# Kernel optimization log

Measured on AMD Instinct MI355X. Metric: run time of the kernel, lower is better.

The kernel has to match this reference:

```python
import jax, jax.numpy as jnp
import numpy as np

N_NODES = 50000
N_EDGES = 400000
IN_DIM = 256
HIDDEN = 256
HEADS = 8
DPH = HIDDEN // HEADS  # 32, out_per_head
OUT_DIM = 128
SEG_EPS = 1e-12   # eps in _segment_softmax
BN_EPS = 1e-5     # torch BatchNorm1d default eps


def _xavier(key, shape):
    fan_in, fan_out = shape[0], shape[-1]
    lim = np.sqrt(6.0 / (fan_in + fan_out))
    return jax.random.uniform(key, shape, jnp.float32, -lim, lim)


def setup_inputs() -> dict:
    key = jax.random.key(0)
    ks = jax.random.split(key, 16)
    x = jax.random.normal(ks[0], (N_NODES, IN_DIM), jnp.float32)
    edge_index = jax.random.randint(ks[1], (2, N_EDGES), 0, N_NODES, jnp.int64)
    return {
        "x": x,
        "edge_index": edge_index,
        # layer 1
        "W1": _xavier(ks[2], (IN_DIM, HIDDEN)),
        "b1": jnp.zeros((HIDDEN,), jnp.float32),
        "a_l1": _xavier(ks[3], (HEADS, DPH)),
        "a_r1": _xavier(ks[4], (HEADS, DPH)),
        "g1": jnp.ones((HIDDEN,), jnp.float32),
        "be1": jnp.zeros((HIDDEN,), jnp.float32),
        # layer 2
        "W2": _xavier(ks[5], (HIDDEN, HIDDEN)),
        "b2": jnp.zeros((HIDDEN,), jnp.float32),
        "a_l2": _xavier(ks[6], (HEADS, DPH)),
        "a_r2": _xavier(ks[7], (HEADS, DPH)),
        "g2": jnp.ones((HIDDEN,), jnp.float32),
        "be2": jnp.zeros((HIDDEN,), jnp.float32),
        # classification head (mlp_hidden=0 -> single Linear)
        "Wh": _xavier(ks[8], (HIDDEN, OUT_DIM)),
        "bh": jnp.zeros((OUT_DIM,), jnp.float32),
    }


def _attn_aggregate(x_proj, src, dst, a_l, a_r):
    """Multi-head GAT aggregation, vectorized over heads.
    x_proj: [N, hidden]; src/dst: [E] int; a_l/a_r: [heads, dph]."""
    N = x_proj.shape[0]
    H = x_proj.reshape(N, HEADS, DPH)
    # per-node score halves (equivalent to (H[src]*a_l).sum + (H[dst]*a_r).sum)
    s_l = jnp.einsum('nhd,hd->nh', H, a_l)  # [N, heads]
    s_r = jnp.einsum('nhd,hd->nh', H, a_r)
    logits = s_l[src] + s_r[dst]            # [E, heads]
    # segment softmax exactly as the source: unstabilized exp + eps denom
    e = jnp.exp(logits)
    denom = jax.ops.segment_sum(e, dst, num_segments=N)       # [N, heads]
    alpha = e / (denom[dst] + SEG_EPS)                         # [E, heads]
    msg = H[src] * alpha[:, :, None]                           # [E, heads, dph]
    out = jax.ops.segment_sum(msg, dst, num_segments=N)        # [N, heads, dph]
    return out.reshape(N, HEADS * DPH)


def _batchnorm(h, gamma, beta):
    # training-mode BatchNorm1d: batch statistics, biased variance
    mean = h.mean(axis=0)
    var = h.var(axis=0)
    return (h - mean) * jax.lax.rsqrt(var + BN_EPS) * gamma + beta


def reference(x, edge_index, W1, b1, a_l1, a_r1, g1, be1,
              W2, b2, a_l2, a_r2, g2, be2, Wh, bh):
    N = x.shape[0]
    # symmetrize edges + add self loops
    ei = jnp.concatenate([edge_index, edge_index[::-1]], axis=1)
    loops = jnp.arange(N, dtype=ei.dtype)
    src = jnp.concatenate([ei[0], loops])
    dst = jnp.concatenate([ei[1], loops])

    x1 = x @ W1 + b1
    x1 = _attn_aggregate(x1, src, dst, a_l1, a_r1)
    x1 = jax.nn.relu(_batchnorm(x1, g1, be1))  # dropout = identity (eval)

    x2 = x1 @ W2 + b2
    x2 = _attn_aggregate(x2, src, dst, a_l2, a_r2)
    x2 = jax.nn.relu(_batchnorm(x2, g2, be2))

    logits = x2 @ Wh + bh  # [N, out_dim]
    return logits
```

## Files before the change

### kernel.cpp

```cpp
#include <hip/hip_runtime.h>
#include <hip/hip_bf16.h>
#include <math.h>

#define NN   50000
#define NE   400000
#define NE2  (2*NE + NN)
#define DIM  256
#define NH   8
#define NM   (NN*DIM)
#define NBLK 196
#define MPAD 50048

typedef __attribute__((ext_vector_type(8))) short bf16x8;
typedef __attribute__((ext_vector_type(4))) float f32x4;

#define GLOAD16(g, l) __builtin_amdgcn_global_load_lds( \
    (const __attribute__((address_space(1))) void*)(g), \
    (__attribute__((address_space(3))) void*)(l), 16, 0, 0)

__device__ __forceinline__ float b2f(unsigned short u) {
    unsigned int i = ((unsigned int)u) << 16;
    float f; __builtin_memcpy(&f, &i, 4); return f;
}
__device__ __forceinline__ unsigned short f2b(float f) {
    __hip_bfloat16 h = __float2bfloat16(f);
    unsigned short u; __builtin_memcpy(&u, &h, 2); return u;
}

__global__ __launch_bounds__(512) void gemm_bf16_wide(
    const unsigned short* __restrict__ A, const unsigned short* __restrict__ Bt,
    const float* __restrict__ bias, unsigned short* __restrict__ Cb)
{
    __shared__ short ldsA[4][128][8];
    __shared__ short ldsB[4][256][8];
    const int tid  = threadIdx.x;
    const int wave = tid >> 6, lane = tid & 63;
    const int wr = wave >> 2, wc = wave & 3;
    const int l15 = lane & 15, lk = lane >> 4;
    const int row0 = blockIdx.x * 128;

    f32x4 acc[4][4] = {};
    for (int k0 = 0; k0 < 256; k0 += 32) {
        GLOAD16(A + (size_t)(row0 + (tid & 127)) * 256 + k0 + (tid >> 7) * 8,
                &ldsA[tid >> 7][tid & 127][0]);
        #pragma unroll
        for (int c = 0; c < 2; ++c) {
            int idx = c * 512 + tid;
            int ch = idx >> 8, r = idx & 255;
            GLOAD16(Bt + (size_t)r * 256 + k0 + ch * 8, &ldsB[ch][r][0]);
        }
        __syncthreads();
        bf16x8 af[4], bf[4];
        #pragma unroll
        for (int m = 0; m < 4; ++m)
            af[m] = *reinterpret_cast<const bf16x8*>(&ldsA[lk][wr*64 + m*16 + l15][0]);
        #pragma unroll
        for (int n = 0; n < 4; ++n)
            bf[n] = *reinterpret_cast<const bf16x8*>(&ldsB[lk][wc*64 + n*16 + l15][0]);
        #pragma unroll
        for (int m = 0; m < 4; ++m)
            #pragma unroll
            for (int n = 0; n < 4; ++n)
                acc[m][n] = __builtin_amdgcn_mfma_f32_16x16x32_bf16(af[m], bf[n], acc[m][n], 0, 0, 0);
        __syncthreads();
    }
    #pragma unroll
    for (int m = 0; m < 4; ++m) {
        #pragma unroll
        for (int n = 0; n < 4; ++n) {
            int col = wc*64 + n*16 + l15;
            float bv = bias[col];
            #pragma unroll
            for (int r = 0; r < 4; ++r) {
                int row = row0 + wr*64 + m*16 + lk*4 + r;
                Cb[(size_t)row * 256 + col] = f2b(acc[m][n][r] + bv);
            }
        }
    }
}

__global__ __launch_bounds__(256) void gemm_bf16_head(
    const unsigned short* __restrict__ A, const unsigned short* __restrict__ Bt,
    const float* __restrict__ bias, float* __restrict__ C)
{
    __shared__ short ldsA[4][128][8];
    __shared__ short ldsB[4][128][8];
    const int tid  = threadIdx.x;
    const int wave = tid >> 6, lane = tid & 63;
    const int wr = wave >> 1, wc = wave & 1;
    const int l15 = lane & 15, lk = lane >> 4;
    const int row0 = blockIdx.x * 128;

    f32x4 acc[4][4] = {};
    for (int k0 = 0; k0 < 256; k0 += 32) {
        #pragma unroll
        for (int c = 0; c < 2; ++c) {
            int idx = c * 256 + tid;
            int ch = idx >> 7, r = idx & 127;
            GLOAD16(A  + (size_t)(row0 + r) * 256 + k0 + ch * 8, &ldsA[ch][r][0]);
            GLOAD16(Bt + (size_t)r * 256 + k0 + ch * 8, &ldsB[ch][r][0]);
        }
        __syncthreads();
        bf16x8 af[4], bf[4];
        #pragma unroll
        for (int m = 0; m < 4; ++m)
            af[m] = *reinterpret_cast<const bf16x8*>(&ldsA[lk][wr*64 + m*16 + l15][0]);
        #pragma unroll
        for (int n = 0; n < 4; ++n)
            bf[n] = *reinterpret_cast<const bf16x8*>(&ldsB[lk][wc*64 + n*16 + l15][0]);
        #pragma unroll
        for (int m = 0; m < 4; ++m)
            #pragma unroll
            for (int n = 0; n < 4; ++n)
                acc[m][n] = __builtin_amdgcn_mfma_f32_16x16x32_bf16(af[m], bf[n], acc[m][n], 0, 0, 0);
        __syncthreads();
    }
    #pragma unroll
    for (int m = 0; m < 4; ++m) {
        #pragma unroll
        for (int n = 0; n < 4; ++n) {
            int col = wc*64 + n*16 + l15;
            float bv = bias[col];
            #pragma unroll
            for (int r = 0; r < 4; ++r) {
                int row = row0 + wr*64 + m*16 + lk*4 + r;
                if (row < NN) C[(size_t)row * 128 + col] = acc[m][n][r] + bv;
            }
        }
    }
}

__global__ __launch_bounds__(256) void cast_x_bf16(
    const float* __restrict__ x, unsigned short* __restrict__ xb)
{
    int idx = blockIdx.x * 256 + threadIdx.x;
    if (idx >= NM / 4) return;
    float4 v = reinterpret_cast<const float4*>(x)[idx];
    ushort4 o = { f2b(v.x), f2b(v.y), f2b(v.z), f2b(v.w) };
    *reinterpret_cast<ushort4*>(&xb[(size_t)idx * 4]) = o;
}

__global__ __launch_bounds__(256) void cast_wt(
    const float* __restrict__ W, unsigned short* __restrict__ Wt, int K, int Nc)
{
    int i = blockIdx.x * 256 + threadIdx.x;
    if (i >= K * Nc) return;
    int k = i / Nc, n = i - k * Nc;
    Wt[n * K + k] = f2b(W[i]);
}

__global__ __launch_bounds__(256) void gat_scores_bf16(
    const unsigned short* __restrict__ Hb, const float* __restrict__ a_l,
    const float* __restrict__ a_r, float* __restrict__ el,
    float* __restrict__ er)
{
    const int wave = threadIdx.x >> 6;
    const int lane = threadIdx.x & 63;
    const int n = blockIdx.x * 4 + wave;
    if (n >= NN) return;
    const int c = lane * 4;
    const int h = lane >> 3;
    ushort4 hv = *reinterpret_cast<const ushort4*>(&Hb[(size_t)n * DIM + c]);
    float4 al4 = *reinterpret_cast<const float4*>(&a_l[c]);
    float4 ar4 = *reinterpret_cast<const float4*>(&a_r[c]);
    float x0 = b2f(hv.x), x1 = b2f(hv.y), x2 = b2f(hv.z), x3 = b2f(hv.w);
    float pl = x0*al4.x + x1*al4.y + x2*al4.z + x3*al4.w;
    float pr = x0*ar4.x + x1*ar4.y + x2*ar4.z + x3*ar4.w;
    #pragma unroll
    for (int o = 1; o < 8; o <<= 1) {
        pl += __shfl_xor(pl, o, 64);
        pr += __shfl_xor(pr, o, 64);
    }
    if ((lane & 7) == 0) {
        el[n * NH + h] = expf(pl);
        er[n * NH + h] = expf(pr);
    }
}

__device__ __forceinline__ void edge_sd(const int* __restrict__ ei, int e2,
                                        int& s, int& d)
{
    if (e2 < NE)          { s = ei[e2];      d = ei[e2 + NE]; }
    else if (e2 < 2 * NE) { s = ei[e2];      d = ei[e2 - NE]; }
    else                  { s = e2 - 2 * NE; d = s; }
}

__global__ __launch_bounds__(256) void deg_count(const int* __restrict__ ei,
                                                 int* __restrict__ deg)
{
    int e2 = blockIdx.x * 256 + threadIdx.x;
    if (e2 >= NE2) return;
    int s, d;
    edge_sd(ei, e2, s, d);
    atomicAdd(&deg[d], 1);
}

__global__ __launch_bounds__(256) void scan_block_sums(
    const int* __restrict__ deg, int* __restrict__ bsum)
{
    __shared__ int tmp[256];
    const int t = threadIdx.x;
    int i = blockIdx.x * 256 + t;
    tmp[t] = (i < NN) ? deg[i] : 0;
    __syncthreads();
    #pragma unroll
    for (int o = 128; o > 0; o >>= 1) {
        if (t < o) tmp[t] += tmp[t + o];
        __syncthreads();
    }
    if (t == 0) bsum[blockIdx.x] = tmp[0];
}

__global__ void scan_bsum(int* __restrict__ bsum)
{
    __shared__ int tmp[256];
    const int t = threadIdx.x;
    int v = (t < NBLK) ? bsum[t] : 0;
    tmp[t] = v;
    __syncthreads();
    #pragma unroll
    for (int o = 1; o < 256; o <<= 1) {
        int x = (t >= o) ? tmp[t - o] : 0;
        __syncthreads();
        tmp[t] += x;
        __syncthreads();
    }
    bsum[t] = tmp[t] - v;
}

__global__ __launch_bounds__(256) void scan_write(
    const int* __restrict__ deg, const int* __restrict__ bsum,
    int* __restrict__ rowoff)
{
    __shared__ int tmp[256];
    const int t = threadIdx.x;
    int i = blockIdx.x * 256 + t;
    int v = (i < NN) ? deg[i] : 0;
    tmp[t] = v;
    __syncthreads();
    #pragma unroll
    for (int o = 1; o < 256; o <<= 1) {
        int x = (t >= o) ? tmp[t - o] : 0;
        __syncthreads();
        tmp[t] += x;
        __syncthreads();
    }
    if (i <= NN) rowoff[i] = bsum[blockIdx.x] + tmp[t] - v;
}

__global__ __launch_bounds__(256) void csr_fill(
    const int* __restrict__ ei, const int* __restrict__ rowoff,
    int* __restrict__ cursor, int* __restrict__ csr)
{
    int e2 = blockIdx.x * 256 + threadIdx.x;
    if (e2 >= NE2) return;
    int s, d;
    edge_sd(ei, e2, s, d);
    int pos = atomicAdd(&cursor[d], 1);
    csr[rowoff[d] + pos] = s;
}

__global__ __launch_bounds__(256) void gat_aggregate_csr_bf16(
    const int* __restrict__ csr, const int* __restrict__ rowoff,
    const unsigned short* __restrict__ Hb, const float* __restrict__ el,
    const float* __restrict__ er, unsigned short* __restrict__ outb)
{
    const int wid  = (blockIdx.x * 256 + threadIdx.x) >> 6;
    const int lane = threadIdx.x & 63;
    if (wid >= NN) return;
    const int h = lane >> 3;
    const int i0 = rowoff[wid], i1 = rowoff[wid + 1];
    const int c4 = lane * 4;

    float ax0 = 0.f, ay0 = 0.f, az0 = 0.f, aw0 = 0.f, den0 = 0.f;
    float ax1 = 0.f, ay1 = 0.f, az1 = 0.f, aw1 = 0.f, den1 = 0.f;

    int i = i0;
    for (; i + 8 <= i1; i += 8) {
        int s[8]; float e[8]; ushort4 hv[8];
        #pragma unroll
        for (int j = 0; j < 8; ++j) s[j] = csr[i + j];
        #pragma unroll
        for (int j = 0; j < 8; ++j) e[j] = el[s[j] * NH + h];
        #pragma unroll
        for (int j = 0; j < 8; ++j)
            hv[j] = *reinterpret_cast<const ushort4*>(&Hb[(size_t)s[j] * DIM + c4]);
        #pragma unroll
        for (int j = 0; j < 8; j += 2) {
            ax0 = fmaf(b2f(hv[j].x), e[j], ax0); ay0 = fmaf(b2f(hv[j].y), e[j], ay0);
            az0 = fmaf(b2f(hv[j].z), e[j], az0); aw0 = fmaf(b2f(hv[j].w), e[j], aw0);
            den0 += e[j];
            ax1 = fmaf(b2f(hv[j+1].x), e[j+1], ax1); ay1 = fmaf(b2f(hv[j+1].y), e[j+1], ay1);
            az1 = fmaf(b2f(hv[j+1].z), e[j+1], az1); aw1 = fmaf(b2f(hv[j+1].w), e[j+1], aw1);
            den1 += e[j+1];
        }
    }
    for (; i + 2 <= i1; i += 2) {
        int s0 = csr[i], s1 = csr[i + 1];
        float e0 = el[s0 * NH + h], e1 = el[s1 * NH + h];
        ushort4 h0 = *reinterpret_cast<const ushort4*>(&Hb[(size_t)s0 * DIM + c4]);
        ushort4 h1 = *reinterpret_cast<const ushort4*>(&Hb[(size_t)s1 * DIM + c4]);
        ax0 = fmaf(b2f(h0.x), e0, ax0); ay0 = fmaf(b2f(h0.y), e0, ay0);
        az0 = fmaf(b2f(h0.z), e0, az0); aw0 = fmaf(b2f(h0.w), e0, aw0);
        den0 += e0;
        ax1 = fmaf(b2f(h1.x), e1, ax1); ay1 = fmaf(b2f(h1.y), e1, ay1);
        az1 = fmaf(b2f(h1.z), e1, az1); aw1 = fmaf(b2f(h1.w), e1, aw1);
        den1 += e1;
    }
    if (i < i1) {
        int s = csr[i];
        float e = el[s * NH + h];
        ushort4 hv = *reinterpret_cast<const ushort4*>(&Hb[(size_t)s * DIM + c4]);
        ax0 = fmaf(b2f(hv.x), e, ax0); ay0 = fmaf(b2f(hv.y), e, ay0);
        az0 = fmaf(b2f(hv.z), e, az0); aw0 = fmaf(b2f(hv.w), e, aw0);
        den0 += e;
    }
    float ax = ax0 + ax1, ay = ay0 + ay1, az = az0 + az1, aw = aw0 + aw1;
    float den = den0 + den1;
    float erv = er[wid * NH + h];
    float inv = erv / fmaf(den, erv, 1e-12f);
    ushort4 r = { f2b(ax * inv), f2b(ay * inv), f2b(az * inv), f2b(aw * inv) };
    *reinterpret_cast<ushort4*>(&outb[(size_t)wid * DIM + c4]) = r;
}

__global__ __launch_bounds__(256) void bn_partial_bf16(
    const unsigned short* __restrict__ H, float* __restrict__ sums)
{
    const int c = threadIdx.x;
    const int r0 = blockIdx.x * 256;
    const int r1 = min(r0 + 256, NN);
    float s = 0.f, q = 0.f;
    for (int r = r0; r < r1; ++r) {
        float v = b2f(H[(size_t)r * DIM + c]);
        s += v;
        q = fmaf(v, v, q);
    }
    atomicAdd(&sums[c], s);
    atomicAdd(&sums[DIM + c], q);
}

__global__ __launch_bounds__(256) void bn_apply_relu_bf16(
    const unsigned short* __restrict__ in, const float* __restrict__ sums,
    const float* __restrict__ g, const float* __restrict__ be,
    unsigned short* __restrict__ out)
{
    __shared__ float sc[DIM], sh[DIM];
    const int t = threadIdx.x;
    {
        float mean = sums[t] * (1.f / NN);
        float var  = sums[DIM + t] * (1.f / NN) - mean * mean;
        float s    = g[t] * rsqrtf(var + 1e-5f);
        sc[t] = s;
        sh[t] = be[t] - mean * s;
    }
    __syncthreads();
    int idx = blockIdx.x * 256 + t;
    if (idx >= NM / 4) return;
    int c4 = (idx & 63) * 4;
    ushort4 v = reinterpret_cast<const ushort4*>(in)[idx];
    ushort4 r = {
        f2b(fmaxf(0.f, fmaf(b2f(v.x), sc[c4 + 0], sh[c4 + 0]))),
        f2b(fmaxf(0.f, fmaf(b2f(v.y), sc[c4 + 1], sh[c4 + 1]))),
        f2b(fmaxf(0.f, fmaf(b2f(v.z), sc[c4 + 2], sh[c4 + 2]))),
        f2b(fmaxf(0.f, fmaf(b2f(v.w), sc[c4 + 3], sh[c4 + 3]))) };
    reinterpret_cast<ushort4*>(out)[idx] = r;
}

extern "C" void kernel_launch(void* const* d_in, const int* in_sizes, int n_in,
                              void* d_out, int out_size, void* d_ws, size_t ws_size,
                              hipStream_t stream)
{
    const float* x   = (const float*)d_in[0];
    const int*   ei  = (const int*)  d_in[1];
    const float* W1  = (const float*)d_in[2];
    const float* b1  = (const float*)d_in[3];
    const float* al1 = (const float*)d_in[4];
    const float* ar1 = (const float*)d_in[5];
    const float* g1  = (const float*)d_in[6];
    const float* be1 = (const float*)d_in[7];
    const float* W2  = (const float*)d_in[8];
    const float* b2  = (const float*)d_in[9];
    const float* al2 = (const float*)d_in[10];
    const float* ar2 = (const float*)d_in[11];
    const float* g2  = (const float*)d_in[12];
    const float* be2 = (const float*)d_in[13];
    const float* Wh  = (const float*)d_in[14];
    const float* bh  = (const float*)d_in[15];
    float* out = (float*)d_out;

    float* ws     = (float*)d_ws;
    float* el     = ws;
    float* er     = el + NN * NH;
    float* bnsum1 = er + NN * NH;
    float* bnsum2 = bnsum1 + 2 * DIM;
    int*   deg    = (int*)(bnsum2 + 2 * DIM);
    int*   cursor = deg + NN;
    int*   rowoff = cursor + NN;
    int*   bsum   = rowoff + NN + 1;
    int*   csr    = bsum + 256;
    unsigned short* xb =
        (unsigned short*)((((uintptr_t)(csr + NE2)) + 63) & ~(uintptr_t)63);
    unsigned short* Hb  = xb  + (size_t)MPAD * 256;
    unsigned short* Ab  = Hb  + (size_t)MPAD * 256;
    unsigned short* Wt1 = Ab  + (size_t)NN * 256;
    unsigned short* Wt2 = Wt1 + 256 * 256;
    unsigned short* Wth = Wt2 + 256 * 256;

    const int gemmBlocks  = MPAD / 128;
    const int edgeBlocks  = (NE2 + 255) / 256;
    const int nodeBlocks  = (NN * 64 + 255) / 256;
    const int bnpBlocks   = (NN + 255) / 256;
    const int elemBlocks  = NM / 4 / 256;

    cast_wt<<<(256 * 256 + 255) / 256, 256, 0, stream>>>(W1, Wt1, 256, 256);
    cast_wt<<<(256 * 256 + 255) / 256, 256, 0, stream>>>(W2, Wt2, 256, 256);
    cast_wt<<<(256 * 128 + 255) / 256, 256, 0, stream>>>(Wh, Wth, 256, 128);
    cast_x_bf16<<<elemBlocks, 256, 0, stream>>>(x, xb);

    hipMemsetAsync(deg, 0, 2 * NN * sizeof(int), stream);
    hipMemsetAsync(bnsum1, 0, 4 * DIM * sizeof(float), stream);

    deg_count<<<edgeBlocks, 256, 0, stream>>>(ei, deg);
    scan_block_sums<<<NBLK, 256, 0, stream>>>(deg, bsum);
    scan_bsum<<<1, 256, 0, stream>>>(bsum);
    scan_write<<<NBLK, 256, 0, stream>>>(deg, bsum, rowoff);
    csr_fill<<<edgeBlocks, 256, 0, stream>>>(ei, rowoff, cursor, csr);

    gemm_bf16_wide<<<gemmBlocks, 512, 0, stream>>>(xb, Wt1, b1, Hb);
    gat_scores_bf16<<<nodeBlocks, 256, 0, stream>>>(Hb, al1, ar1, el, er);
    gat_aggregate_csr_bf16<<<nodeBlocks, 256, 0, stream>>>(csr, rowoff, Hb, el, er, Ab);
    bn_partial_bf16<<<bnpBlocks, 256, 0, stream>>>(Ab, bnsum1);
    bn_apply_relu_bf16<<<elemBlocks, 256, 0, stream>>>(Ab, bnsum1, g1, be1, xb);

    gemm_bf16_wide<<<gemmBlocks, 512, 0, stream>>>(xb, Wt2, b2, Hb);
    gat_scores_bf16<<<nodeBlocks, 256, 0, stream>>>(Hb, al2, ar2, el, er);
    gat_aggregate_csr_bf16<<<nodeBlocks, 256, 0, stream>>>(csr, rowoff, Hb, el, er, Ab);
    bn_partial_bf16<<<bnpBlocks, 256, 0, stream>>>(Ab, bnsum2);
    bn_apply_relu_bf16<<<elemBlocks, 256, 0, stream>>>(Ab, bnsum2, g2, be2, xb);

    gemm_bf16_head<<<gemmBlocks, 256, 0, stream>>>(xb, Wth, bh, out);
}
```

Measured before the change: 502.2 us.

## Fuse input cast and BatchNorm-ReLU into GEMM A-tile loads

The fp32-to-bf16 cast of x now happens inside the first GEMM's A-tile load. The BatchNorm scale/shift plus ReLU is applied while loading A in the second GEMM and in the head GEMM, so the standalone cast and bn_apply kernels and their full-size intermediate buffers go away. The three weight-cast launches are merged into one kernel, and the aggregate loop's unroll drops from 8 to 4. In exchange, A loads become synchronous register loads instead of async global-to-LDS copies, and the Ab buffer grows to MPAD rows so padded rows can be read.

```diff
diff --git a/kernel.cpp b/kernel.cpp
--- a/kernel.cpp
+++ b/kernel.cpp
@@ -12,6 +12,7 @@
 #define MPAD 50048
 
 typedef __attribute__((ext_vector_type(8))) short bf16x8;
+typedef __attribute__((ext_vector_type(8))) unsigned short u16x8;
 typedef __attribute__((ext_vector_type(4))) float f32x4;
 
 #define GLOAD16(g, l) __builtin_amdgcn_global_load_lds( \
@@ -27,27 +28,69 @@
     unsigned short u; __builtin_memcpy(&u, &h, 2); return u;
 }
 
-__global__ __launch_bounds__(512) void gemm_bf16_wide(
-    const unsigned short* __restrict__ A, const unsigned short* __restrict__ Bt,
-    const float* __restrict__ bias, unsigned short* __restrict__ Cb)
+template<int MODE>
+__global__ __launch_bounds__(512) void gemm_wide(
+    const float* __restrict__ Af, const unsigned short* __restrict__ Ab16,
+    const unsigned short* __restrict__ Bt, const float* __restrict__ bias,
+    const float* __restrict__ sums, const float* __restrict__ g,
+    const float* __restrict__ be, unsigned short* __restrict__ Cb)
 {
     __shared__ short ldsA[4][128][8];
     __shared__ short ldsB[4][256][8];
+    __shared__ float scL[256], shL[256];
     const int tid  = threadIdx.x;
     const int wave = tid >> 6, lane = tid & 63;
     const int wr = wave >> 2, wc = wave & 3;
     const int l15 = lane & 15, lk = lane >> 4;
     const int row0 = blockIdx.x * 128;
 
+    if (MODE == 1) {
+        if (tid < 256) {
+            float mean = sums[tid] * (1.f / NN);
+            float var  = sums[256 + tid] * (1.f / NN) - mean * mean;
+            float s    = g[tid] * rsqrtf(var + 1e-5f);
+            scL[tid] = s;
+            shL[tid] = be[tid] - mean * s;
+        }
+        __syncthreads();
+    }
+
+    const int r  = tid & 127, ch = tid >> 7;
+    const size_t arow = (MODE == 0) ? (size_t)min(row0 + r, NN - 1)
+                                    : (size_t)(row0 + r);
+
     f32x4 acc[4][4] = {};
-    for (int k0 = 0; k0 < 256; k0 += 32) {
-        GLOAD16(A + (size_t)(row0 + (tid & 127)) * 256 + k0 + (tid >> 7) * 8,
-                &ldsA[tid >> 7][tid & 127][0]);
+    for (int t = 0; t < 8; ++t) {
+        const int k0 = t * 32, kc = k0 + ch * 8;
+        if (t) __syncthreads();
+        u16x8 o;
+        if (MODE == 0) {
+            const float* p = Af + arow * 256 + kc;
+            float4 v0 = *reinterpret_cast<const float4*>(p);
+            float4 v1 = *reinterpret_cast<const float4*>(p + 4);
+            o[0]=f2b(v0.x); o[1]=f2b(v0.y); o[2]=f2b(v0.z); o[3]=f2b(v0.w);
+            o[4]=f2b(v1.x); o[5]=f2b(v1.y); o[6]=f2b(v1.z); o[7]=f2b(v1.w);
+        } else {
+            u16x8 rw = *reinterpret_cast<const u16x8*>(Ab16 + arow * 256 + kc);
+            float4 s0 = *reinterpret_cast<const float4*>(&scL[kc]);
+            float4 s1 = *reinterpret_cast<const float4*>(&scL[kc + 4]);
+            float4 h0 = *reinterpret_cast<const float4*>(&shL[kc]);
+            float4 h1 = *reinterpret_cast<const float4*>(&shL[kc + 4]);
+            o[0]=f2b(fmaxf(0.f, fmaf(b2f(rw[0]), s0.x, h0.x)));
+            o[1]=f2b(fmaxf(0.f, fmaf(b2f(rw[1]), s0.y, h0.y)));
+            o[2]=f2b(fmaxf(0.f, fmaf(b2f(rw[2]), s0.z, h0.z)));
+            o[3]=f2b(fmaxf(0.f, fmaf(b2f(rw[3]), s0.w, h0.w)));
+            o[4]=f2b(fmaxf(0.f, fmaf(b2f(rw[4]), s1.x, h1.x)));
+            o[5]=f2b(fmaxf(0.f, fmaf(b2f(rw[5]), s1.y, h1.y)));
+            o[6]=f2b(fmaxf(0.f, fmaf(b2f(rw[6]), s1.z, h1.z)));
+            o[7]=f2b(fmaxf(0.f, fmaf(b2f(rw[7]), s1.w, h1.w)));
+        }
+        *reinterpret_cast<u16x8*>(&ldsA[ch][r][0]) = o;
         #pragma unroll
         for (int c = 0; c < 2; ++c) {
             int idx = c * 512 + tid;
-            int ch = idx >> 8, r = idx & 255;
-            GLOAD16(Bt + (size_t)r * 256 + k0 + ch * 8, &ldsB[ch][r][0]);
+            int bch = idx >> 8, br = idx & 255;
+            GLOAD16(Bt + (size_t)br * 256 + k0 + bch * 8, &ldsB[bch][br][0]);
         }
         __syncthreads();
         bf16x8 af[4], bf[4];
@@ -62,7 +105,6 @@
             #pragma unroll
             for (int n = 0; n < 4; ++n)
                 acc[m][n] = __builtin_amdgcn_mfma_f32_16x16x32_bf16(af[m], bf[n], acc[m][n], 0, 0, 0);
-        __syncthreads();
     }
     #pragma unroll
     for (int m = 0; m < 4; ++m) {
@@ -71,34 +113,64 @@
             int col = wc*64 + n*16 + l15;
             float bv = bias[col];
             #pragma unroll
-            for (int r = 0; r < 4; ++r) {
-                int row = row0 + wr*64 + m*16 + lk*4 + r;
-                Cb[(size_t)row * 256 + col] = f2b(acc[m][n][r] + bv);
+            for (int q = 0; q < 4; ++q) {
+                int row = row0 + wr*64 + m*16 + lk*4 + q;
+                Cb[(size_t)row * 256 + col] = f2b(acc[m][n][q] + bv);
             }
         }
     }
 }
 
-__global__ __launch_bounds__(256) void gemm_bf16_head(
-    const unsigned short* __restrict__ A, const unsigned short* __restrict__ Bt,
-    const float* __restrict__ bias, float* __restrict__ C)
+__global__ __launch_bounds__(256) void gemm_head(
+    const unsigned short* __restrict__ Ab16, const unsigned short* __restrict__ Bt,
+    const float* __restrict__ bias, const float* __restrict__ sums,
+    const float* __restrict__ g, const float* __restrict__ be,
+    float* __restrict__ C)
 {
     __shared__ short ldsA[4][128][8];
     __shared__ short ldsB[4][128][8];
+    __shared__ float scL[256], shL[256];
     const int tid  = threadIdx.x;
     const int wave = tid >> 6, lane = tid & 63;
     const int wr = wave >> 1, wc = wave & 1;
     const int l15 = lane & 15, lk = lane >> 4;
     const int row0 = blockIdx.x * 128;
 
+    {
+        float mean = sums[tid] * (1.f / NN);
+        float var  = sums[256 + tid] * (1.f / NN) - mean * mean;
+        float s    = g[tid] * rsqrtf(var + 1e-5f);
+        scL[tid] = s;
+        shL[tid] = be[tid] - mean * s;
+    }
+    __syncthreads();
+
     f32x4 acc[4][4] = {};
-    for (int k0 = 0; k0 < 256; k0 += 32) {
+    for (int t = 0; t < 8; ++t) {
+        const int k0 = t * 32;
+        if (t) __syncthreads();
         #pragma unroll
         for (int c = 0; c < 2; ++c) {
             int idx = c * 256 + tid;
             int ch = idx >> 7, r = idx & 127;
-            GLOAD16(A  + (size_t)(row0 + r) * 256 + k0 + ch * 8, &ldsA[ch][r][0]);
-            GLOAD16(Bt + (size_t)r * 256 + k0 + ch * 8, &ldsB[ch][r][0]);
+            int kc = k0 + ch * 8;
+            u16x8 rw = *reinterpret_cast<const u16x8*>(
+                Ab16 + (size_t)(row0 + r) * 256 + kc);
+            float4 s0 = *reinterpret_cast<const float4*>(&scL[kc]);
+            float4 s1 = *reinterpret_cast<const float4*>(&scL[kc + 4]);
+            float4 h0 = *reinterpret_cast<const float4*>(&shL[kc]);
+            float4 h1 = *reinterpret_cast<const float4*>(&shL[kc + 4]);
+            u16x8 o;
+            o[0]=f2b(fmaxf(0.f, fmaf(b2f(rw[0]), s0.x, h0.x)));
+            o[1]=f2b(fmaxf(0.f, fmaf(b2f(rw[1]), s0.y, h0.y)));
+            o[2]=f2b(fmaxf(0.f, fmaf(b2f(rw[2]), s0.z, h0.z)));
+            o[3]=f2b(fmaxf(0.f, fmaf(b2f(rw[3]), s0.w, h0.w)));
+            o[4]=f2b(fmaxf(0.f, fmaf(b2f(rw[4]), s1.x, h1.x)));
+            o[5]=f2b(fmaxf(0.f, fmaf(b2f(rw[5]), s1.y, h1.y)));
+            o[6]=f2b(fmaxf(0.f, fmaf(b2f(rw[6]), s1.z, h1.z)));
+            o[7]=f2b(fmaxf(0.f, fmaf(b2f(rw[7]), s1.w, h1.w)));
+            *reinterpret_cast<u16x8*>(&ldsA[ch][r][0]) = o;
+            GLOAD16(Bt + (size_t)r * 256 + kc, &ldsB[ch][r][0]);
         }
         __syncthreads();
         bf16x8 af[4], bf[4];
@@ -113,7 +185,6 @@
             #pragma unroll
             for (int n = 0; n < 4; ++n)
                 acc[m][n] = __builtin_amdgcn_mfma_f32_16x16x32_bf16(af[m], bf[n], acc[m][n], 0, 0, 0);
-        __syncthreads();
     }
     #pragma unroll
     for (int m = 0; m < 4; ++m) {
@@ -122,31 +193,29 @@
             int col = wc*64 + n*16 + l15;
             float bv = bias[col];
             #pragma unroll
-            for (int r = 0; r < 4; ++r) {
-                int row = row0 + wr*64 + m*16 + lk*4 + r;
-                if (row < NN) C[(size_t)row * 128 + col] = acc[m][n][r] + bv;
+            for (int q = 0; q < 4; ++q) {
+                int row = row0 + wr*64 + m*16 + lk*4 + q;
+                if (row < NN) C[(size_t)row * 128 + col] = acc[m][n][q] + bv;
             }
         }
     }
 }
 
-__global__ __launch_bounds__(256) void cast_x_bf16(
-    const float* __restrict__ x, unsigned short* __restrict__ xb)
-{
-    int idx = blockIdx.x * 256 + threadIdx.x;
-    if (idx >= NM / 4) return;
-    float4 v = reinterpret_cast<const float4*>(x)[idx];
-    ushort4 o = { f2b(v.x), f2b(v.y), f2b(v.z), f2b(v.w) };
-    *reinterpret_cast<ushort4*>(&xb[(size_t)idx * 4]) = o;
-}
-
-__global__ __launch_bounds__(256) void cast_wt(
-    const float* __restrict__ W, unsigned short* __restrict__ Wt, int K, int Nc)
+__global__ __launch_bounds__(256) void cast_wt_all(
+    const float* __restrict__ W1, const float* __restrict__ W2,
+    const float* __restrict__ Wh, unsigned short* __restrict__ Wt1,
+    unsigned short* __restrict__ Wt2, unsigned short* __restrict__ Wth)
 {
     int i = blockIdx.x * 256 + threadIdx.x;
-    if (i >= K * Nc) return;
-    int k = i / Nc, n = i - k * Nc;
-    Wt[n * K + k] = f2b(W[i]);
+    {
+        int k = i >> 8, n = i & 255;
+        Wt1[n * 256 + k] = f2b(W1[i]);
+        Wt2[n * 256 + k] = f2b(W2[i]);
+    }
+    if (i < 256 * 128) {
+        int k = i >> 7, n = i & 127;
+        Wth[n * 256 + k] = f2b(Wh[i]);
+    }
 }
 
 __global__ __launch_bounds__(256) void gat_scores_bf16(
@@ -276,38 +345,28 @@
     float ax1 = 0.f, ay1 = 0.f, az1 = 0.f, aw1 = 0.f, den1 = 0.f;
 
     int i = i0;
-    for (; i + 8 <= i1; i += 8) {
-        int s[8]; float e[8]; ushort4 hv[8];
-        #pragma unroll
-        for (int j = 0; j < 8; ++j) s[j] = csr[i + j];
-        #pragma unroll
-        for (int j = 0; j < 8; ++j) e[j] = el[s[j] * NH + h];
-        #pragma unroll
-        for (int j = 0; j < 8; ++j)
-            hv[j] = *reinterpret_cast<const ushort4*>(&Hb[(size_t)s[j] * DIM + c4]);
-        #pragma unroll
-        for (int j = 0; j < 8; j += 2) {
-            ax0 = fmaf(b2f(hv[j].x), e[j], ax0); ay0 = fmaf(b2f(hv[j].y), e[j], ay0);
-            az0 = fmaf(b2f(hv[j].z), e[j], az0); aw0 = fmaf(b2f(hv[j].w), e[j], aw0);
-            den0 += e[j];
-            ax1 = fmaf(b2f(hv[j+1].x), e[j+1], ax1); ay1 = fmaf(b2f(hv[j+1].y), e[j+1], ay1);
-            az1 = fmaf(b2f(hv[j+1].z), e[j+1], az1); aw1 = fmaf(b2f(hv[j+1].w), e[j+1], aw1);
-            den1 += e[j+1];
-        }
-    }
-    for (; i + 2 <= i1; i += 2) {
-        int s0 = csr[i], s1 = csr[i + 1];
+    for (; i + 4 <= i1; i += 4) {
+        int s0 = csr[i + 0], s1 = csr[i + 1], s2 = csr[i + 2], s3 = csr[i + 3];
         float e0 = el[s0 * NH + h], e1 = el[s1 * NH + h];
+        float e2 = el[s2 * NH + h], e3 = el[s3 * NH + h];
         ushort4 h0 = *reinterpret_cast<const ushort4*>(&Hb[(size_t)s0 * DIM + c4]);
         ushort4 h1 = *reinterpret_cast<const ushort4*>(&Hb[(size_t)s1 * DIM + c4]);
+        ushort4 h2 = *reinterpret_cast<const ushort4*>(&Hb[(size_t)s2 * DIM + c4]);
+        ushort4 h3 = *reinterpret_cast<const ushort4*>(&Hb[(size_t)s3 * DIM + c4]);
         ax0 = fmaf(b2f(h0.x), e0, ax0); ay0 = fmaf(b2f(h0.y), e0, ay0);
         az0 = fmaf(b2f(h0.z), e0, az0); aw0 = fmaf(b2f(h0.w), e0, aw0);
         den0 += e0;
         ax1 = fmaf(b2f(h1.x), e1, ax1); ay1 = fmaf(b2f(h1.y), e1, ay1);
         az1 = fmaf(b2f(h1.z), e1, az1); aw1 = fmaf(b2f(h1.w), e1, aw1);
         den1 += e1;
-    }
-    if (i < i1) {
+        ax0 = fmaf(b2f(h2.x), e2, ax0); ay0 = fmaf(b2f(h2.y), e2, ay0);
+        az0 = fmaf(b2f(h2.z), e2, az0); aw0 = fmaf(b2f(h2.w), e2, aw0);
+        den0 += e2;
+        ax1 = fmaf(b2f(h3.x), e3, ax1); ay1 = fmaf(b2f(h3.y), e3, ay1);
+        az1 = fmaf(b2f(h3.z), e3, az1); aw1 = fmaf(b2f(h3.w), e3, aw1);
+        den1 += e3;
+    }
+    for (; i < i1; ++i) {
         int s = csr[i];
         float e = el[s * NH + h];
         ushort4 hv = *reinterpret_cast<const ushort4*>(&Hb[(size_t)s * DIM + c4]);
@@ -337,33 +396,6 @@
     }
     atomicAdd(&sums[c], s);
     atomicAdd(&sums[DIM + c], q);
-}
-
-__global__ __launch_bounds__(256) void bn_apply_relu_bf16(
-    const unsigned short* __restrict__ in, const float* __restrict__ sums,
-    const float* __restrict__ g, const float* __restrict__ be,
-    unsigned short* __restrict__ out)
-{
-    __shared__ float sc[DIM], sh[DIM];
-    const int t = threadIdx.x;
-    {
-        float mean = sums[t] * (1.f / NN);
-        float var  = sums[DIM + t] * (1.f / NN) - mean * mean;
-        float s    = g[t] * rsqrtf(var + 1e-5f);
-        sc[t] = s;
-        sh[t] = be[t] - mean * s;
-    }
-    __syncthreads();
-    int idx = blockIdx.x * 256 + t;
-    if (idx >= NM / 4) return;
-    int c4 = (idx & 63) * 4;
-    ushort4 v = reinterpret_cast<const ushort4*>(in)[idx];
-    ushort4 r = {
-        f2b(fmaxf(0.f, fmaf(b2f(v.x), sc[c4 + 0], sh[c4 + 0]))),
-        f2b(fmaxf(0.f, fmaf(b2f(v.y), sc[c4 + 1], sh[c4 + 1]))),
-        f2b(fmaxf(0.f, fmaf(b2f(v.z), sc[c4 + 2], sh[c4 + 2]))),
-        f2b(fmaxf(0.f, fmaf(b2f(v.w), sc[c4 + 3], sh[c4 + 3]))) };
-    reinterpret_cast<ushort4*>(out)[idx] = r;
 }
 
 extern "C" void kernel_launch(void* const* d_in, const int* in_sizes, int n_in,
@@ -398,11 +430,10 @@
     int*   rowoff = cursor + NN;
     int*   bsum   = rowoff + NN + 1;
     int*   csr    = bsum + 256;
-    unsigned short* xb =
+    unsigned short* Hb =
         (unsigned short*)((((uintptr_t)(csr + NE2)) + 63) & ~(uintptr_t)63);
-    unsigned short* Hb  = xb  + (size_t)MPAD * 256;
     unsigned short* Ab  = Hb  + (size_t)MPAD * 256;
-    unsigned short* Wt1 = Ab  + (size_t)NN * 256;
+    unsigned short* Wt1 = Ab  + (size_t)MPAD * 256;
     unsigned short* Wt2 = Wt1 + 256 * 256;
     unsigned short* Wth = Wt2 + 256 * 256;
 
@@ -410,13 +441,8 @@
     const int edgeBlocks  = (NE2 + 255) / 256;
     const int nodeBlocks  = (NN * 64 + 255) / 256;
     const int bnpBlocks   = (NN + 255) / 256;
-    const int elemBlocks  = NM / 4 / 256;
-
-    cast_wt<<<(256 * 256 + 255) / 256, 256, 0, stream>>>(W1, Wt1, 256, 256);
-    cast_wt<<<(256 * 256 + 255) / 256, 256, 0, stream>>>(W2, Wt2, 256, 256);
-    cast_wt<<<(256 * 128 + 255) / 256, 256, 0, stream>>>(Wh, Wth, 256, 128);
-    cast_x_bf16<<<elemBlocks, 256, 0, stream>>>(x, xb);
-
+
+    cast_wt_all<<<256, 256, 0, stream>>>(W1, W2, Wh, Wt1, Wt2, Wth);
     hipMemsetAsync(deg, 0, 2 * NN * sizeof(int), stream);
     hipMemsetAsync(bnsum1, 0, 4 * DIM * sizeof(float), stream);
 
@@ -426,17 +452,17 @@
     scan_write<<<NBLK, 256, 0, stream>>>(deg, bsum, rowoff);
     csr_fill<<<edgeBlocks, 256, 0, stream>>>(ei, rowoff, cursor, csr);
 
-    gemm_bf16_wide<<<gemmBlocks, 512, 0, stream>>>(xb, Wt1, b1, Hb);
+    gemm_wide<0><<<gemmBlocks, 512, 0, stream>>>(x, nullptr, Wt1, b1,
+                                                 nullptr, nullptr, nullptr, Hb);
     gat_scores_bf16<<<nodeBlocks, 256, 0, stream>>>(Hb, al1, ar1, el, er);
     gat_aggregate_csr_bf16<<<nodeBlocks, 256, 0, stream>>>(csr, rowoff, Hb, el, er, Ab);
     bn_partial_bf16<<<bnpBlocks, 256, 0, stream>>>(Ab, bnsum1);
-    bn_apply_relu_bf16<<<elemBlocks, 256, 0, stream>>>(Ab, bnsum1, g1, be1, xb);
-
-    gemm_bf16_wide<<<gemmBlocks, 512, 0, stream>>>(xb, Wt2, b2, Hb);
+
+    gemm_wide<1><<<gemmBlocks, 512, 0, stream>>>(nullptr, Ab, Wt2, b2,
+                                                 bnsum1, g1, be1, Hb);
     gat_scores_bf16<<<nodeBlocks, 256, 0, stream>>>(Hb, al2, ar2, el, er);
     gat_aggregate_csr_bf16<<<nodeBlocks, 256, 0, stream>>>(csr, rowoff, Hb, el, er, Ab);
     bn_partial_bf16<<<bnpBlocks, 256, 0, stream>>>(Ab, bnsum2);
-    bn_apply_relu_bf16<<<elemBlocks, 256, 0, stream>>>(Ab, bnsum2, g2, be2, xb);
-
-    gemm_bf16_head<<<gemmBlocks, 256, 0, stream>>>(xb, Wth, bh, out);
-}
+
+    gemm_head<<<gemmBlocks, 256, 0, stream>>>(Ab, Wth, bh, bnsum2, g2, be2, out);
+}
```

After: 489.1 us. -2.6%, faster.
